# Optimization experiments

Hardware: AMD Instinct MI355X
Metric: run time of the kernel (lower is better)

## Reference

```python
import jax, jax.numpy as jnp
import numpy as np

H = 4
NEG_SLOPE = 0.2
N_P, N_A = 100000, 100000
E = 500000
L = 200000
F_IN, F_HID, F_OUT = 128, 128, 64


def setup_inputs() -> dict:
    key = jax.random.key(0)
    ks = jax.random.split(key, 32)
    s = 0.1  # weight init scale
    inp = {
        'x_paper': jax.random.normal(ks[0], (N_P, F_IN), jnp.float32),
        'x_author': jax.random.normal(ks[1], (N_A, F_IN), jnp.float32),
        'ei_pa': jax.random.randint(ks[2], (2, E), 0, N_P, jnp.int32),
        'ei_ap': jax.random.randint(ks[3], (2, E), 0, N_A, jnp.int32),
        'edge_label_index': jax.random.randint(ks[4], (2, L), 0, N_P, jnp.int32),
        # layer 1 params
        'p1W': s * jax.random.normal(ks[5], (F_IN, F_HID), jnp.float32),
        'p1b': jnp.zeros((F_HID,), jnp.float32),
        'a1W': s * jax.random.normal(ks[6], (F_IN, F_HID), jnp.float32),
        'a1b': jnp.zeros((F_HID,), jnp.float32),
        's1pa': s * jax.random.normal(ks[7], (H, F_HID // H), jnp.float32),
        'd1pa': s * jax.random.normal(ks[8], (H, F_HID // H), jnp.float32),
        's1ap': s * jax.random.normal(ks[9], (H, F_HID // H), jnp.float32),
        'd1ap': s * jax.random.normal(ks[10], (H, F_HID // H), jnp.float32),
        'k1W': s * jax.random.normal(ks[11], (F_HID, F_HID), jnp.float32),
        'k1b': jnp.zeros((F_HID,), jnp.float32),
        'q1': s * jax.random.normal(ks[12], (F_HID,), jnp.float32),
        # layer 2 params
        'p2W': s * jax.random.normal(ks[13], (F_HID, F_OUT), jnp.float32),
        'p2b': jnp.zeros((F_OUT,), jnp.float32),
        'a2W': s * jax.random.normal(ks[14], (F_HID, F_OUT), jnp.float32),
        'a2b': jnp.zeros((F_OUT,), jnp.float32),
        's2pa': s * jax.random.normal(ks[15], (H, F_OUT // H), jnp.float32),
        'd2pa': s * jax.random.normal(ks[16], (H, F_OUT // H), jnp.float32),
        's2ap': s * jax.random.normal(ks[17], (H, F_OUT // H), jnp.float32),
        'd2ap': s * jax.random.normal(ks[18], (H, F_OUT // H), jnp.float32),
        'k2W': s * jax.random.normal(ks[19], (F_OUT, F_OUT), jnp.float32),
        'k2b': jnp.zeros((F_OUT,), jnp.float32),
        'q2': s * jax.random.normal(ks[20], (F_OUT,), jnp.float32),
    }
    return inp


def _edge_attn(h_src, h_dst, src, dst, a_src, a_dst, num_dst):
    # h_*: [N, H, D]; a_*: [H, D]. Per-edge node-level GAT-style attention.
    alpha = (jnp.einsum('nhd,hd->nh', h_src, a_src)[src]
             + jnp.einsum('nhd,hd->nh', h_dst, a_dst)[dst])  # [E, H]
    alpha = jnp.where(alpha >= 0, alpha, NEG_SLOPE * alpha)  # leaky_relu
    amax = jax.ops.segment_max(alpha, dst, num_segments=num_dst)
    amax = jnp.where(jnp.isfinite(amax), amax, 0.0)
    ex = jnp.exp(alpha - amax[dst])
    denom = jax.ops.segment_sum(ex, dst, num_segments=num_dst)
    w = ex / (denom[dst] + 1e-16)
    out = jax.ops.segment_sum(h_src[src] * w[:, :, None], dst, num_segments=num_dst)
    return jax.nn.relu(out).reshape(num_dst, -1)  # [N_dst, H*D]


def _group(xs, q, kW, kb):
    # Semantic-level attention over metapaths (PyG HANConv `group`).
    out = jnp.stack(xs)  # [M, N, F]
    score = (q * jnp.tanh(out @ kW + kb).mean(axis=1)).sum(-1)  # [M]
    attn = jax.nn.softmax(score)
    return (attn[:, None, None] * out).sum(0)


def _han_layer(x_p, x_a, ei_pa, ei_ap, pW, pb, aW, ab, s_pa, d_pa, s_ap, d_ap, kW, kb, q):
    D = pW.shape[1] // H
    h_p = (x_p @ pW + pb).reshape(-1, H, D)
    h_a = (x_a @ aW + ab).reshape(-1, H, D)
    out_a = _edge_attn(h_p, h_a, ei_pa[0], ei_pa[1], s_pa, d_pa, h_a.shape[0])
    out_p = _edge_attn(h_a, h_p, ei_ap[0], ei_ap[1], s_ap, d_ap, h_p.shape[0])
    z_p = _group([out_p], q, kW, kb)
    z_a = _group([out_a], q, kW, kb)
    return z_p, z_a


def reference(x_paper, x_author, ei_pa, ei_ap, edge_label_index,
              p1W, p1b, a1W, a1b, s1pa, d1pa, s1ap, d1ap, k1W, k1b, q1,
              p2W, p2b, a2W, a2b, s2pa, d2pa, s2ap, d2ap, k2W, k2b, q2):
    z_p, z_a = _han_layer(x_paper, x_author, ei_pa, ei_ap,
                          p1W, p1b, a1W, a1b, s1pa, d1pa, s1ap, d1ap, k1W, k1b, q1)
    z_p, z_a = _han_layer(z_p, z_a, ei_pa, ei_ap,
                          p2W, p2b, a2W, a2b, s2pa, d2pa, s2ap, d2ap, k2W, k2b, q2)
    src = z_p[edge_label_index[0]]
    dst = z_a[edge_label_index[1]]
    return (src * dst).sum(axis=-1)  # [L]
```

## Files before the change

kernel.cpp:

```cpp
#include <hip/hip_runtime.h>


#define HEADS 4

typedef _Float16 f16x8 __attribute__((ext_vector_type(8)));
typedef _Float16 f16x4 __attribute__((ext_vector_type(4)));
typedef float    f32x4 __attribute__((ext_vector_type(4)));

__device__ __forceinline__ float leaky02(float a) {
    return a >= 0.f ? a : 0.2f * a;
}

__device__ __forceinline__ void prep_one(const float* W, _Float16* Wf, int M, int o) {
    const int NT = M / 16;
    const int v = o & 7, lane = (o >> 3) & 63, jt = o >> 9;
    const int t = jt / NT, j = jt % NT;
    const int k = t * 32 + (lane >> 4) * 8 + v;
    const int n = j * 16 + (lane & 15);
    Wf[o] = (_Float16)W[k * M + n];
}

__global__ __launch_bounds__(256) void prep_w4(
    const float* __restrict__ W1, _Float16* __restrict__ Wf1,
    const float* __restrict__ W2, _Float16* __restrict__ Wf2,
    const float* __restrict__ W3, _Float16* __restrict__ Wf3,
    const float* __restrict__ W4, _Float16* __restrict__ Wf4) {
    int o = blockIdx.x * 256 + threadIdx.x;
    if (o < 16384)       prep_one(W1, Wf1, 128, o);
    else if (o < 32768)  prep_one(W2, Wf2, 128, o - 16384);
    else if (o < 40960)  prep_one(W3, Wf3, 64, o - 32768);
    else if (o < 49152)  prep_one(W4, Wf4, 64, o - 40960);
}

template<int M, bool AHALF>
__global__ __launch_bounds__(256) void gemm_mfma_dual(
    const void* __restrict__ XA, const _Float16* __restrict__ WfA,
    const float* __restrict__ bA, _Float16* __restrict__ outA,
    const float* __restrict__ svA, const float* __restrict__ dvA,
    float* __restrict__ asA, float* __restrict__ adA,
    const void* __restrict__ XB, const _Float16* __restrict__ WfB,
    const float* __restrict__ bB, _Float16* __restrict__ outB,
    const float* __restrict__ svB, const float* __restrict__ dvB,
    float* __restrict__ asB, float* __restrict__ adB,
    int N, int nbHalf) {
    constexpr int NT  = M / 16;
    constexpr int D   = M / HEADS;
    constexpr int SA  = 136;
    constexpr int SE  = M + 4;
    constexpr int WFH = NT * 4 * 64 * 8;
    __shared__ _Float16 lds_a[64 * SA];
    __shared__ _Float16 lds_w[WFH];

    const bool second = blockIdx.x >= nbHalf;
    const void* __restrict__ X      = second ? XB : XA;
    const _Float16* __restrict__ Wf = second ? WfB : WfA;
    const float* __restrict__ b     = second ? bB : bA;
    _Float16* __restrict__ out      = second ? outB : outA;
    const float* __restrict__ sv    = second ? svB : svA;
    const float* __restrict__ dv    = second ? dvB : dvA;
    float* __restrict__ asb         = second ? asB : asA;
    float* __restrict__ adb         = second ? adB : adA;
    const int brow = second ? blockIdx.x - nbHalf : blockIdx.x;

    const int wave = threadIdx.x >> 6;
    const int lane = threadIdx.x & 63;
    const int row0 = brow * 64;
    const int m    = lane & 15;
    const int quad = lane >> 4;

    {
        const int base = threadIdx.x * 8;
        #pragma unroll
        for (int it = 0; it < WFH / 2048; ++it) {
            f16x8 v = *(const f16x8*)(Wf + it * 2048 + base);
            *(f16x8*)(lds_w + it * 2048 + base) = v;
        }
    }
    if (AHALF) {
        #pragma unroll
        for (int it = 0; it < 4; ++it) {
            const int r = it * 16 + (threadIdx.x >> 4);
            const int k = (threadIdx.x & 15) * 8;
            int gr = row0 + r; if (gr >= N) gr = N - 1;
            f16x8 v = *(const f16x8*)((const _Float16*)X + (size_t)gr * 128 + k);
            *(f16x8*)(lds_a + r * SA + k) = v;
        }
    } else {
        #pragma unroll
        for (int it = 0; it < 8; ++it) {
            const int r = it * 8 + (threadIdx.x >> 5);
            const int k = (threadIdx.x & 31) * 4;
            int gr = row0 + r; if (gr >= N) gr = N - 1;
            float4 v = *(const float4*)((const float*)X + (size_t)gr * 128 + k);
            f16x4 h = {(_Float16)v.x, (_Float16)v.y, (_Float16)v.z, (_Float16)v.w};
            *(f16x4*)(lds_a + r * SA + k) = h;
        }
    }
    __syncthreads();

    f32x4 acc[NT];
    #pragma unroll
    for (int j = 0; j < NT; ++j) acc[j] = (f32x4){0.f, 0.f, 0.f, 0.f};

    const int ab = (wave * 16 + m) * SA;
    #pragma unroll
    for (int t = 0; t < 4; ++t) {
        f16x8 a = *(const f16x8*)(lds_a + ab + t * 32 + quad * 8);
        #pragma unroll
        for (int j = 0; j < NT; ++j) {
            f16x8 bf = *(const f16x8*)(lds_w + ((t * NT + j) * 64 + lane) * 8);
            acc[j] = __builtin_amdgcn_mfma_f32_16x16x32_f16(a, bf, acc[j], 0, 0, 0);
        }
    }
    __syncthreads();

    #pragma unroll
    for (int j = 0; j < NT; ++j) {
        const float bias = b[j * 16 + m];
        #pragma unroll
        for (int r = 0; r < 4; ++r)
            lds_a[(wave * 16 + quad * 4 + r) * SE + j * 16 + m] =
                (_Float16)(acc[j][r] + bias);
    }

    {
        const int r  = lane >> 2;
        const int hh = lane & 3;
        float ps = 0.f, pd = 0.f;
        #pragma unroll
        for (int j = 0; j < D / 4; ++j) {
            f16x4 v4 = *(const f16x4*)(&lds_a[(wave * 16 + r) * SE + hh * D + 4 * j]);
            float4 s4 = *(const float4*)(sv + hh * D + 4 * j);
            float4 d4 = *(const float4*)(dv + hh * D + 4 * j);
            const float v0 = (float)v4[0], v1 = (float)v4[1],
                        v2 = (float)v4[2], v3 = (float)v4[3];
            ps += v0 * s4.x + v1 * s4.y + v2 * s4.z + v3 * s4.w;
            pd += v0 * d4.x + v1 * d4.y + v2 * d4.z + v3 * d4.w;
        }
        const int grow = row0 + wave * 16 + r;
        if (grow < N) {
            asb[(size_t)grow * HEADS + hh] = ps;
            adb[(size_t)grow * HEADS + hh] = pd;
        }
    }

    constexpr int LPR = M / 4;
    constexpr int RPI = 64 / LPR;
    const int lr = lane % LPR;
    const int rq = lane / LPR;
    #pragma unroll
    for (int i = 0; i < 16 / RPI; ++i) {
        const int rr = wave * 16 + i * RPI + rq;
        const int grow = row0 + rr;
        if (grow < N) {
            f16x4 v = *(const f16x4*)(&lds_a[rr * SE + lr * 4]);
            *(f16x4*)(out + (size_t)grow * M + lr * 4) = v;
        }
    }
}

__global__ __launch_bounds__(256) void hist_dual(
    const int* __restrict__ dst_pa, const int* __restrict__ dst_ap,
    int* __restrict__ counts, int N, int E) {
    const int eg = blockIdx.x * 256 + threadIdx.x;
    if (eg >= 2 * E) return;
    const int idx = (eg < E) ? dst_pa[eg] : (N + dst_ap[eg - E]);
    atomicAdd(counts + idx, 1);
}

__global__ __launch_bounds__(256) void scan_blk(
    const int* __restrict__ in, int* __restrict__ out,
    int* __restrict__ bsum, int N) {
    __shared__ int sh[256];
    const int base = blockIdx.x * 1024 + threadIdx.x * 4;
    int v[4]; int s = 0;
    #pragma unroll
    for (int j = 0; j < 4; ++j) { v[j] = (base + j < N) ? in[base + j] : 0; s += v[j]; }
    sh[threadIdx.x] = s;
    __syncthreads();
    for (int off = 1; off < 256; off <<= 1) {
        int t = (threadIdx.x >= off) ? sh[threadIdx.x - off] : 0;
        __syncthreads();
        sh[threadIdx.x] += t;
        __syncthreads();
    }
    int run = sh[threadIdx.x] - s;
    #pragma unroll
    for (int j = 0; j < 4; ++j) {
        if (base + j < N) out[base + j] = run;
        run += v[j];
    }
    if (threadIdx.x == 255) bsum[blockIdx.x] = sh[255];
}

__global__ __launch_bounds__(256) void scan_sums(int* __restrict__ bsum, int nb) {
    __shared__ int sh[256];
    int v = (threadIdx.x < nb) ? bsum[threadIdx.x] : 0;
    sh[threadIdx.x] = v;
    __syncthreads();
    for (int off = 1; off < 256; off <<= 1) {
        int t = (threadIdx.x >= off) ? sh[threadIdx.x - off] : 0;
        __syncthreads();
        sh[threadIdx.x] += t;
        __syncthreads();
    }
    if (threadIdx.x < nb) bsum[threadIdx.x] = sh[threadIdx.x] - v;
}

__global__ __launch_bounds__(256) void scan_add(
    int* __restrict__ out, const int* __restrict__ bsum, int N) {
    const int base = blockIdx.x * 1024 + threadIdx.x * 4;
    const int add = bsum[blockIdx.x];
    #pragma unroll
    for (int j = 0; j < 4; ++j)
        if (base + j < N) out[base + j] += add;
}

__global__ __launch_bounds__(256) void scatter_dual(
    const int* __restrict__ src_pa, const int* __restrict__ dst_pa,
    const int* __restrict__ src_ap, const int* __restrict__ dst_ap,
    const int* __restrict__ offsets, int* __restrict__ cursor,
    int* __restrict__ perm, int N, int E) {
    const int eg = blockIdx.x * 256 + threadIdx.x;
    if (eg >= 2 * E) return;
    int idx, val;
    if (eg < E) { idx = dst_pa[eg];         val = src_pa[eg]; }
    else        { idx = N + dst_ap[eg - E]; val = src_ap[eg - E]; }
    const int pos = offsets[idx] + atomicAdd(cursor + idx, 1);
    perm[pos] = val;
}

__global__ __launch_bounds__(256) void deg_hist(
    const int* __restrict__ cnt, int* __restrict__ bhist, int n) {
    __shared__ int lh[64];
    if (threadIdx.x < 64) lh[threadIdx.x] = 0;
    __syncthreads();
    for (int i = blockIdx.x * 256 + threadIdx.x; i < n; i += gridDim.x * 256) {
        int c = cnt[i]; if (c > 63) c = 63;
        atomicAdd(&lh[c], 1);
    }
    __syncthreads();
    if (threadIdx.x < 64) atomicAdd(&bhist[threadIdx.x], lh[threadIdx.x]);
}

__global__ __launch_bounds__(256) void deg_scatter(
    const int* __restrict__ cnt, int* __restrict__ bcur,
    int* __restrict__ order, int n) {
    __shared__ int lh[64];
    __shared__ int lbase[64];
    if (threadIdx.x < 64) lh[threadIdx.x] = 0;
    __syncthreads();
    const int i = blockIdx.x * 256 + threadIdx.x;
    int c = 0, lpos = 0;
    if (i < n) {
        c = cnt[i]; if (c > 63) c = 63;
        lpos = atomicAdd(&lh[c], 1);
    }
    __syncthreads();
    if (threadIdx.x < 64 && lh[threadIdx.x] > 0)
        lbase[threadIdx.x] = atomicAdd(&bcur[threadIdx.x], lh[threadIdx.x]);
    __syncthreads();
    if (i < n) order[lbase[c] + lpos] = i;
}

template<int F, int D>
__global__ __launch_bounds__(256) void csr_attn_agg_dual(
    const int* __restrict__ order,
    const int* __restrict__ perm, const int* __restrict__ offsets,
    const int* __restrict__ counts,
    const float* __restrict__ asrcP, const float* __restrict__ adstP,
    const _Float16* __restrict__ hP, _Float16* __restrict__ outA,
    const float* __restrict__ asrcA, const float* __restrict__ adstA,
    const _Float16* __restrict__ hA, _Float16* __restrict__ outP,
    int N) {
    constexpr int LPN = F / 8;
    const int gid  = blockIdx.x * 256 + threadIdx.x;
    const int slot = gid / LPN;
    const int lane = gid % LPN;
    if (slot >= 2 * N) return;
    const int node_g = order[slot];
    const bool second = node_g >= N;
    const int node = second ? node_g - N : node_g;
    const float* __restrict__ asrc    = second ? asrcA : asrcP;
    const float* __restrict__ adst    = second ? adstA : adstP;
    const _Float16* __restrict__ hsrc = second ? hA : hP;
    _Float16* __restrict__ out        = second ? outP : outA;

    const int start = offsets[node_g];
    const int cnt   = counts[node_g];
    const int f0 = lane * 8;
    const int h  = f0 / D;
    const float ad = adst[(size_t)node * HEADS + h];

    float den = 0.f;
    float acc[8];
    #pragma unroll
    for (int j = 0; j < 8; ++j) acc[j] = 0.f;
    int i = 0;
    for (; i + 4 <= cnt; i += 4) {
        const int s0 = perm[start + i + 0];
        const int s1 = perm[start + i + 1];
        const int s2 = perm[start + i + 2];
        const int s3 = perm[start + i + 3];
        const float a0 = asrc[(size_t)s0 * HEADS + h];
        const float a1 = asrc[(size_t)s1 * HEADS + h];
        const float a2 = asrc[(size_t)s2 * HEADS + h];
        const float a3 = asrc[(size_t)s3 * HEADS + h];
        f16x8 h0 = *(const f16x8*)(hsrc + (size_t)s0 * F + f0);
        f16x8 h1 = *(const f16x8*)(hsrc + (size_t)s1 * F + f0);
        f16x8 h2 = *(const f16x8*)(hsrc + (size_t)s2 * F + f0);
        f16x8 h3 = *(const f16x8*)(hsrc + (size_t)s3 * F + f0);
        const float e0 = __expf(leaky02(a0 + ad));
        const float e1 = __expf(leaky02(a1 + ad));
        const float e2 = __expf(leaky02(a2 + ad));
        const float e3 = __expf(leaky02(a3 + ad));
        den += (e0 + e1) + (e2 + e3);
        #pragma unroll
        for (int j = 0; j < 8; ++j)
            acc[j] += e0 * (float)h0[j] + e1 * (float)h1[j]
                    + e2 * (float)h2[j] + e3 * (float)h3[j];
    }
    for (; i < cnt; ++i) {
        const int s = perm[start + i];
        const float a = leaky02(asrc[(size_t)s * HEADS + h] + ad);
        const float ex = __expf(a);
        den += ex;
        f16x8 hv = *(const f16x8*)(hsrc + (size_t)s * F + f0);
        #pragma unroll
        for (int j = 0; j < 8; ++j)
            acc[j] += ex * (float)hv[j];
    }
    const float inv = 1.f / (den + 1e-16f);
    f16x8 o;
    #pragma unroll
    for (int j = 0; j < 8; ++j)
        o[j] = (_Float16)fmaxf(acc[j] * inv, 0.f);
    *(f16x8*)(out + (size_t)node * F + f0) = o;
}

__global__ __launch_bounds__(256) void edge_dot(
    const int* __restrict__ eli, const _Float16* __restrict__ zp,
    const _Float16* __restrict__ za, float* __restrict__ out, int L) {
    constexpr int LPE = 8;
    const int gid  = blockIdx.x * blockDim.x + threadIdx.x;
    const int e    = gid / LPE;
    const int lane = gid % LPE;
    if (e >= L) return;
    const int p = eli[e], a = eli[(size_t)L + e];
    f16x8 pv = *(const f16x8*)(zp + (size_t)p * 64 + lane * 8);
    f16x8 av = *(const f16x8*)(za + (size_t)a * 64 + lane * 8);
    float s = 0.f;
    #pragma unroll
    for (int j = 0; j < 8; ++j) s += (float)pv[j] * (float)av[j];
    #pragma unroll
    for (int off = 4; off > 0; off >>= 1) s += __shfl_xor(s, off);
    if (lane == 0) out[e] = s;
}

static inline int cdiv(long long a, long long b) { return (int)((a + b - 1) / b); }

extern "C" void kernel_launch(void* const* d_in, const int* in_sizes, int n_in,
                              void* d_out, int out_size, void* d_ws, size_t ws_size,
                              hipStream_t stream) {
    const float* x_p  = (const float*)d_in[0];
    const float* x_a  = (const float*)d_in[1];
    const int* ei_pa  = (const int*)d_in[2];
    const int* ei_ap  = (const int*)d_in[3];
    const int* eli    = (const int*)d_in[4];
    const float* p1W = (const float*)d_in[5];
    const float* p1b = (const float*)d_in[6];
    const float* a1W = (const float*)d_in[7];
    const float* a1b = (const float*)d_in[8];
    const float* s1pa = (const float*)d_in[9];
    const float* d1pa = (const float*)d_in[10];
    const float* s1ap = (const float*)d_in[11];
    const float* d1ap = (const float*)d_in[12];
    const float* p2W = (const float*)d_in[16];
    const float* p2b = (const float*)d_in[17];
    const float* a2W = (const float*)d_in[18];
    const float* a2b = (const float*)d_in[19];
    const float* s2pa = (const float*)d_in[20];
    const float* d2pa = (const float*)d_in[21];
    const float* s2ap = (const float*)d_in[22];
    const float* d2ap = (const float*)d_in[23];

    const int NP = in_sizes[0] / 128;
    const int E  = in_sizes[2] / 2;
    const int L  = in_sizes[4] / 2;
    const int N  = NP;

    char* ws = (char*)d_ws;
    size_t off = 0;
    auto alloc = [&](size_t bytes) -> char* {
        char* p = ws + off;
        off += (bytes + 255) & ~(size_t)255;
        return p;
    };
    _Float16* h_p1   = (_Float16*)alloc((size_t)N * 128 * 2);
    _Float16* h_a1   = (_Float16*)alloc((size_t)N * 128 * 2);
    _Float16* out_p1 = (_Float16*)alloc((size_t)N * 128 * 2);
    _Float16* out_a1 = (_Float16*)alloc((size_t)N * 128 * 2);
    _Float16* h_p2   = (_Float16*)alloc((size_t)N * 64 * 2);
    _Float16* h_a2   = (_Float16*)alloc((size_t)N * 64 * 2);
    _Float16* out_p2 = (_Float16*)alloc((size_t)N * 64 * 2);
    _Float16* out_a2 = (_Float16*)alloc((size_t)N * 64 * 2);
    float* asrc_pa = (float*)alloc((size_t)N * HEADS * 4);
    float* adst_pa = (float*)alloc((size_t)N * HEADS * 4);
    float* asrc_ap = (float*)alloc((size_t)N * HEADS * 4);
    float* adst_ap = (float*)alloc((size_t)N * HEADS * 4);
    _Float16* Wf1p = (_Float16*)alloc(16384 * 2);
    _Float16* Wf1a = (_Float16*)alloc(16384 * 2);
    _Float16* Wf2p = (_Float16*)alloc(8192 * 2);
    _Float16* Wf2a = (_Float16*)alloc(8192 * 2);
    int* cnt2    = (int*)alloc((size_t)2 * N * 4);
    int* cursor2 = (int*)alloc((size_t)2 * N * 4);
    int* bhist   = (int*)alloc(256);
    int* off2    = (int*)alloc((size_t)2 * N * 4);
    int* perm2   = (int*)alloc((size_t)2 * E * 4);
    int* order2  = (int*)alloc((size_t)2 * N * 4);
    int* bsum    = (int*)alloc(256 * 4);

    const int* src_pa = ei_pa;
    const int* dst_pa = ei_pa + E;
    const int* src_ap = ei_ap;
    const int* dst_ap = ei_ap + E;

    const int N2 = 2 * N;
    const int nbScan = cdiv(N2, 1024);

    prep_w4<<<cdiv(49152, 256), 256, 0, stream>>>(p1W, Wf1p, a1W, Wf1a, p2W, Wf2p, a2W, Wf2a);
    hipMemsetAsync(cnt2, 0, ((size_t)4 * N + 64) * 4, stream);
    hist_dual<<<cdiv((long long)2 * E, 256), 256, 0, stream>>>(dst_pa, dst_ap, cnt2, N, E);
    scan_blk<<<nbScan, 256, 0, stream>>>(cnt2, off2, bsum, N2);
    scan_sums<<<1, 256, 0, stream>>>(bsum, nbScan);
    scan_add<<<nbScan, 256, 0, stream>>>(off2, bsum, N2);
    scatter_dual<<<cdiv((long long)2 * E, 256), 256, 0, stream>>>(
        src_pa, dst_pa, src_ap, dst_ap, off2, cursor2, perm2, N, E);
    deg_hist<<<256, 256, 0, stream>>>(cnt2, bhist, N2);
    scan_sums<<<1, 256, 0, stream>>>(bhist, 64);
    deg_scatter<<<cdiv(N2, 256), 256, 0, stream>>>(cnt2, bhist, order2, N2);

    const int nbHalf = cdiv(N, 64);

    gemm_mfma_dual<128, false><<<2 * nbHalf, 256, 0, stream>>>(
        x_p, Wf1p, p1b, h_p1, s1pa, d1ap, asrc_pa, adst_ap,
        x_a, Wf1a, a1b, h_a1, s1ap, d1pa, asrc_ap, adst_pa, N, nbHalf);
    csr_attn_agg_dual<128, 32><<<cdiv((long long)N2 * 16, 256), 256, 0, stream>>>(
        order2, perm2, off2, cnt2,
        asrc_pa, adst_pa, h_p1, out_a1,
        asrc_ap, adst_ap, h_a1, out_p1, N);

    gemm_mfma_dual<64, true><<<2 * nbHalf, 256, 0, stream>>>(
        out_p1, Wf2p, p2b, h_p2, s2pa, d2ap, asrc_pa, adst_ap,
        out_a1, Wf2a, a2b, h_a2, s2ap, d2pa, asrc_ap, adst_pa, N, nbHalf);
    csr_attn_agg_dual<64, 16><<<cdiv((long long)N2 * 8, 256), 256, 0, stream>>>(
        order2, perm2, off2, cnt2,
        asrc_pa, adst_pa, h_p2, out_a2,
        asrc_ap, adst_ap, h_a2, out_p2, N);

    edge_dot<<<cdiv((long long)L * 8, 256), 256, 0, stream>>>(
        eli, out_p2, out_a2, (float*)d_out, L);
}
```

Measured before the change: 449.3 us.

## Split 128-wide GEMM output columns across two blocks to shrink LDS and registers

The first-layer GEMM now launches two blocks per 64-row tile, each computing 64 output columns. The weight prep layout is regrouped so each block loads only its half of the fragments. Attention logits are computed per half, with a shuffle reduction when a head spans 32 columns. The epilogue reuses the A tile stride and drops a barrier. This lowers per-block LDS and accumulator registers to raise occupancy, at the cost of loading and converting the fp32 X tile twice.

```diff
diff --git a/kernel.cpp b/kernel.cpp
--- a/kernel.cpp
+++ b/kernel.cpp
@@ -12,11 +12,10 @@
 }
 
 __device__ __forceinline__ void prep_one(const float* W, _Float16* Wf, int M, int o) {
-    const int NT = M / 16;
-    const int v = o & 7, lane = (o >> 3) & 63, jt = o >> 9;
-    const int t = jt / NT, j = jt % NT;
+    const int v = o & 7, lane = (o >> 3) & 63, rest = o >> 9;
+    const int jl = rest & 3, t = (rest >> 2) & 3, grp = rest >> 4;
     const int k = t * 32 + (lane >> 4) * 8 + v;
-    const int n = j * 16 + (lane & 15);
+    const int n = (grp * 4 + jl) * 16 + (lane & 15);
     Wf[o] = (_Float16)W[k * M + n];
 }
 
@@ -42,16 +41,18 @@
     const float* __restrict__ bB, _Float16* __restrict__ outB,
     const float* __restrict__ svB, const float* __restrict__ dvB,
     float* __restrict__ asB, float* __restrict__ adB,
-    int N, int nbHalf) {
-    constexpr int NT  = M / 16;
+    int N, int nbs) {
+    constexpr int NSPLIT = (M == 128) ? 2 : 1;
+    constexpr int JT  = 4;
     constexpr int D   = M / HEADS;
+    constexpr int HPB = 64 / D;
+    constexpr int HL  = 4 / HPB;
     constexpr int SA  = 136;
-    constexpr int SE  = M + 4;
-    constexpr int WFH = NT * 4 * 64 * 8;
+    constexpr int WFH = JT * 4 * 64 * 8;
     __shared__ _Float16 lds_a[64 * SA];
     __shared__ _Float16 lds_w[WFH];
 
-    const bool second = blockIdx.x >= nbHalf;
+    const bool second = blockIdx.x >= (unsigned)nbs;
     const void* __restrict__ X      = second ? XB : XA;
     const _Float16* __restrict__ Wf = second ? WfB : WfA;
     const float* __restrict__ b     = second ? bB : bA;
@@ -60,19 +61,23 @@
     const float* __restrict__ dv    = second ? dvB : dvA;
     float* __restrict__ asb         = second ? asB : asA;
     float* __restrict__ adb         = second ? adB : adA;
-    const int brow = second ? blockIdx.x - nbHalf : blockIdx.x;
+    const int b0    = second ? blockIdx.x - nbs : blockIdx.x;
+    const int brow  = b0 / NSPLIT;
+    const int split = b0 % NSPLIT;
+    const int row0  = brow * 64;
+    const int colb  = split * 64;
 
     const int wave = threadIdx.x >> 6;
     const int lane = threadIdx.x & 63;
-    const int row0 = brow * 64;
     const int m    = lane & 15;
     const int quad = lane >> 4;
 
     {
+        const _Float16* wsrc = Wf + split * WFH;
         const int base = threadIdx.x * 8;
         #pragma unroll
         for (int it = 0; it < WFH / 2048; ++it) {
-            f16x8 v = *(const f16x8*)(Wf + it * 2048 + base);
+            f16x8 v = *(const f16x8*)(wsrc + it * 2048 + base);
             *(f16x8*)(lds_w + it * 2048 + base) = v;
         }
     }
@@ -98,63 +103,64 @@
     }
     __syncthreads();
 
-    f32x4 acc[NT];
-    #pragma unroll
-    for (int j = 0; j < NT; ++j) acc[j] = (f32x4){0.f, 0.f, 0.f, 0.f};
+    f32x4 acc[JT];
+    #pragma unroll
+    for (int j = 0; j < JT; ++j) acc[j] = (f32x4){0.f, 0.f, 0.f, 0.f};
 
     const int ab = (wave * 16 + m) * SA;
     #pragma unroll
     for (int t = 0; t < 4; ++t) {
         f16x8 a = *(const f16x8*)(lds_a + ab + t * 32 + quad * 8);
         #pragma unroll
-        for (int j = 0; j < NT; ++j) {
-            f16x8 bf = *(const f16x8*)(lds_w + ((t * NT + j) * 64 + lane) * 8);
+        for (int j = 0; j < JT; ++j) {
+            f16x8 bf = *(const f16x8*)(lds_w + ((t * JT + j) * 64 + lane) * 8);
             acc[j] = __builtin_amdgcn_mfma_f32_16x16x32_f16(a, bf, acc[j], 0, 0, 0);
         }
     }
-    __syncthreads();
-
-    #pragma unroll
-    for (int j = 0; j < NT; ++j) {
-        const float bias = b[j * 16 + m];
+
+    #pragma unroll
+    for (int j = 0; j < JT; ++j) {
+        const float bias = b[colb + j * 16 + m];
         #pragma unroll
         for (int r = 0; r < 4; ++r)
-            lds_a[(wave * 16 + quad * 4 + r) * SE + j * 16 + m] =
+            lds_a[(wave * 16 + quad * 4 + r) * SA + j * 16 + m] =
                 (_Float16)(acc[j][r] + bias);
     }
 
     {
-        const int r  = lane >> 2;
-        const int hh = lane & 3;
+        const int r = lane >> 2;
+        const int q = lane & 3;
         float ps = 0.f, pd = 0.f;
         #pragma unroll
-        for (int j = 0; j < D / 4; ++j) {
-            f16x4 v4 = *(const f16x4*)(&lds_a[(wave * 16 + r) * SE + hh * D + 4 * j]);
-            float4 s4 = *(const float4*)(sv + hh * D + 4 * j);
-            float4 d4 = *(const float4*)(dv + hh * D + 4 * j);
+        for (int j = 0; j < 4; ++j) {
+            f16x4 v4 = *(const f16x4*)(&lds_a[(wave * 16 + r) * SA + q * 16 + 4 * j]);
+            float4 s4 = *(const float4*)(sv + colb + q * 16 + 4 * j);
+            float4 d4 = *(const float4*)(dv + colb + q * 16 + 4 * j);
             const float v0 = (float)v4[0], v1 = (float)v4[1],
                         v2 = (float)v4[2], v3 = (float)v4[3];
             ps += v0 * s4.x + v1 * s4.y + v2 * s4.z + v3 * s4.w;
             pd += v0 * d4.x + v1 * d4.y + v2 * d4.z + v3 * d4.w;
         }
+        if (HL == 2) { ps += __shfl_xor(ps, 1); pd += __shfl_xor(pd, 1); }
         const int grow = row0 + wave * 16 + r;
-        if (grow < N) {
+        if (grow < N && (q & (HL - 1)) == 0) {
+            const int hh = split * HPB + q / HL;
             asb[(size_t)grow * HEADS + hh] = ps;
             adb[(size_t)grow * HEADS + hh] = pd;
         }
     }
 
-    constexpr int LPR = M / 4;
-    constexpr int RPI = 64 / LPR;
-    const int lr = lane % LPR;
-    const int rq = lane / LPR;
-    #pragma unroll
-    for (int i = 0; i < 16 / RPI; ++i) {
-        const int rr = wave * 16 + i * RPI + rq;
-        const int grow = row0 + rr;
-        if (grow < N) {
-            f16x4 v = *(const f16x4*)(&lds_a[rr * SE + lr * 4]);
-            *(f16x4*)(out + (size_t)grow * M + lr * 4) = v;
+    {
+        const int lr = lane & 15;
+        const int rq = lane >> 4;
+        #pragma unroll
+        for (int i = 0; i < 4; ++i) {
+            const int lrow = i * 4 + rq;
+            const int grow = row0 + wave * 16 + lrow;
+            if (grow < N) {
+                f16x4 v = *(const f16x4*)(&lds_a[(wave * 16 + lrow) * SA + lr * 4]);
+                *(f16x4*)(out + (size_t)grow * M + colb + lr * 4) = v;
+            }
         }
     }
 }
@@ -440,19 +446,20 @@
     scan_sums<<<1, 256, 0, stream>>>(bhist, 64);
     deg_scatter<<<cdiv(N2, 256), 256, 0, stream>>>(cnt2, bhist, order2, N2);
 
-    const int nbHalf = cdiv(N, 64);
-
-    gemm_mfma_dual<128, false><<<2 * nbHalf, 256, 0, stream>>>(
+    const int nbs1 = cdiv(N, 64) * 2;
+    const int nbs2 = cdiv(N, 64);
+
+    gemm_mfma_dual<128, false><<<2 * nbs1, 256, 0, stream>>>(
         x_p, Wf1p, p1b, h_p1, s1pa, d1ap, asrc_pa, adst_ap,
-        x_a, Wf1a, a1b, h_a1, s1ap, d1pa, asrc_ap, adst_pa, N, nbHalf);
+        x_a, Wf1a, a1b, h_a1, s1ap, d1pa, asrc_ap, adst_pa, N, nbs1);
     csr_attn_agg_dual<128, 32><<<cdiv((long long)N2 * 16, 256), 256, 0, stream>>>(
         order2, perm2, off2, cnt2,
         asrc_pa, adst_pa, h_p1, out_a1,
         asrc_ap, adst_ap, h_a1, out_p1, N);
 
-    gemm_mfma_dual<64, true><<<2 * nbHalf, 256, 0, stream>>>(
+    gemm_mfma_dual<64, true><<<2 * nbs2, 256, 0, stream>>>(
         out_p1, Wf2p, p2b, h_p2, s2pa, d2ap, asrc_pa, adst_ap,
-        out_a1, Wf2a, a2b, h_a2, s2ap, d2pa, asrc_ap, adst_pa, N, nbHalf);
+        out_a1, Wf2a, a2b, h_a2, s2ap, d2pa, asrc_ap, adst_pa, N, nbs2);
     csr_attn_agg_dual<64, 16><<<cdiv((long long)N2 * 8, 256), 256, 0, stream>>>(
         order2, perm2, off2, cnt2,
         asrc_pa, adst_pa, h_p2, out_a2,
```

Measured after the change: 439.9 us. 1.02x faster.
